# Performance work log

Hardware: AMD Instinct MI355X
Metric: run time of the kernel (lower is better)

The kernel has to match this reference:

```python
import jax, jax.numpy as jnp
import numpy as np

SIZE_IN = 4096
SIZE_OUT = 4096
STEPS = 8  # single-int steps variant of SparseLayer
BATCH = 8192


def _build_mask(size_in, size_out, steps):
    # Replicates the single-int `steps` branch of SparseLayer.__init__:
    # row i has ones at columns k*inp_el_counts + (i % inp_el_counts), k in [0, steps)
    inp_el_counts = size_in // steps
    rows = np.arange(size_out)
    count = rows % inp_el_counts                      # [size_out]
    cols = (np.arange(steps)[None, :] * inp_el_counts + count[:, None])  # [size_out, steps]
    mask = np.zeros((size_out, size_in), dtype=np.float32)
    mask[rows[:, None], cols] = 1.0
    return mask


def setup_inputs() -> dict:
    key = jax.random.key(0)
    kx, kw, kb = jax.random.split(key, 3)
    x = jax.random.normal(kx, (BATCH, SIZE_IN), dtype=jnp.float32)
    # kaiming_uniform_(a=sqrt(5)) -> uniform(-b, b) with b = sqrt(6/((1+5)*fan_in)) = 1/sqrt(fan_in)
    bound = 1.0 / np.sqrt(SIZE_IN)
    weights = jax.random.uniform(kw, (SIZE_OUT, SIZE_IN), minval=-bound, maxval=bound, dtype=jnp.float32)
    bias = jax.random.uniform(kb, (SIZE_OUT,), minval=-bound, maxval=bound, dtype=jnp.float32)
    mask = jnp.asarray(_build_mask(SIZE_IN, SIZE_OUT, STEPS))
    return {"x": x, "weights": weights, "bias": bias, "mask": mask}


def reference(x, weights, bias, mask):
    # out = x @ (W * mask)^T + b  ; mask is a fixed structured-sparsity pattern
    w = weights * mask                                  # [size_out, size_in]
    return jnp.einsum('bi,oi->bo', x, w) + bias         # [B, size_out]
```

## Files before the change

kernel.cpp:

```cpp
#include <hip/hip_runtime.h>

#define SIZE_IN   4096
#define SIZE_OUT  4096
#define STEPS     8
#define IEC       512
#define GROUPS    8
#define BATCH     8192

#define C0_TILE         128
#define ROWS_PER_BLOCK  8
#define THREADS         256

__global__ void sparse_compress_w(const float* __restrict__ W, float* __restrict__ wc) {
    int idx = blockIdx.x * blockDim.x + threadIdx.x;
    int c0 = idx & (IEC - 1);
    int k  = (idx >> 9) & (STEPS - 1);
    int g  = idx >> 12;
    int row = g * IEC + c0;
    int col = k * IEC + c0;
    wc[idx] = W[(size_t)row * SIZE_IN + col];
}

__global__ __launch_bounds__(THREADS) void sparse_mm(
        const float* __restrict__ x, const float* __restrict__ wc,
        const float* __restrict__ bias, float* __restrict__ out) {
    __shared__ float lw[GROUPS * STEPS * C0_TILE];
    const int bx  = blockIdx.x;
    const int by  = blockIdx.y;
    const int tid = threadIdx.x;

    const float4* wc4 = (const float4*)wc;
    float4*       lw4 = (float4*)lw;
    #pragma unroll
    for (int i = 0; i < 8; ++i) {
        int flat4 = i * THREADS + tid;
        int gk = flat4 >> 5;
        int c4 = flat4 & 31;
        lw4[flat4] = wc4[gk * (IEC / 4) + bx * (C0_TILE / 4) + c4];
    }
    __syncthreads();

    const int r    = tid >> 5;
    const int lane = tid & 31;
    const int b    = by * ROWS_PER_BLOCK + r;
    const int c0   = bx * C0_TILE + lane * 4;

    const float4* xrow = (const float4*)(x + (size_t)b * SIZE_IN);
    float4 xv[STEPS];
    #pragma unroll
    for (int k = 0; k < STEPS; ++k)
        xv[k] = xrow[(k * IEC + c0) >> 2];

    float4*       orow = (float4*)(out + (size_t)b * SIZE_OUT);
    const float4* b4   = (const float4*)bias;
    #pragma unroll
    for (int g = 0; g < GROUPS; ++g) {
        float4 acc = b4[(g * IEC + c0) >> 2];
        #pragma unroll
        for (int k = 0; k < STEPS; ++k) {
            const float4 w = *(const float4*)&lw[(g * STEPS + k) * C0_TILE + lane * 4];
            acc.x += xv[k].x * w.x;
            acc.y += xv[k].y * w.y;
            acc.z += xv[k].z * w.z;
            acc.w += xv[k].w * w.w;
        }
        orow[(g * IEC + c0) >> 2] = acc;
    }
}

extern "C" void kernel_launch(void* const* d_in, const int* in_sizes, int n_in,
                              void* d_out, int out_size, void* d_ws, size_t ws_size,
                              hipStream_t stream) {
    const float* x    = (const float*)d_in[0];
    const float* W    = (const float*)d_in[1];
    const float* bias = (const float*)d_in[2];
    float* out = (float*)d_out;
    float* wc  = (float*)d_ws;

    hipLaunchKernelGGL(sparse_compress_w,
                       dim3(GROUPS * STEPS * IEC / 256), dim3(256), 0, stream, W, wc);

    dim3 grid(IEC / C0_TILE, BATCH / ROWS_PER_BLOCK);
    hipLaunchKernelGGL(sparse_mm, grid, dim3(THREADS), 0, stream, x, wc, bias, out);
}
```

Baseline: 50.34 us.

## Make sparse_mm persistent over batch chunks and use nontemporal output stores

New measurement: 54.10 us. 1.07x slower.

```diff
diff --git a/kernel.cpp b/kernel.cpp
--- a/kernel.cpp
+++ b/kernel.cpp
@@ -10,6 +10,9 @@
 #define C0_TILE         128
 #define ROWS_PER_BLOCK  8
 #define THREADS         256
+#define GRID_Y          256
+
+typedef float f4 __attribute__((ext_vector_type(4)));
 
 __global__ void sparse_compress_w(const float* __restrict__ W, float* __restrict__ wc) {
     int idx = blockIdx.x * blockDim.x + threadIdx.x;
@@ -24,13 +27,11 @@
 __global__ __launch_bounds__(THREADS) void sparse_mm(
         const float* __restrict__ x, const float* __restrict__ wc,
         const float* __restrict__ bias, float* __restrict__ out) {
-    __shared__ float lw[GROUPS * STEPS * C0_TILE];
+    __shared__ f4 lw4[GROUPS * STEPS * (C0_TILE / 4)];
     const int bx  = blockIdx.x;
-    const int by  = blockIdx.y;
     const int tid = threadIdx.x;
 
-    const float4* wc4 = (const float4*)wc;
-    float4*       lw4 = (float4*)lw;
+    const f4* wc4 = (const f4*)wc;
     #pragma unroll
     for (int i = 0; i < 8; ++i) {
         int flat4 = i * THREADS + tid;
@@ -38,33 +39,37 @@
         int c4 = flat4 & 31;
         lw4[flat4] = wc4[gk * (IEC / 4) + bx * (C0_TILE / 4) + c4];
     }
-    __syncthreads();
 
     const int r    = tid >> 5;
     const int lane = tid & 31;
-    const int b    = by * ROWS_PER_BLOCK + r;
-    const int c0   = bx * C0_TILE + lane * 4;
 
-    const float4* xrow = (const float4*)(x + (size_t)b * SIZE_IN);
-    float4 xv[STEPS];
+    const f4* b4 = (const f4*)bias;
+    f4 bv[GROUPS];
     #pragma unroll
-    for (int k = 0; k < STEPS; ++k)
-        xv[k] = xrow[(k * IEC + c0) >> 2];
+    for (int g = 0; g < GROUPS; ++g)
+        bv[g] = b4[(g * IEC + bx * C0_TILE) / 4 + lane];
 
-    float4*       orow = (float4*)(out + (size_t)b * SIZE_OUT);
-    const float4* b4   = (const float4*)bias;
-    #pragma unroll
-    for (int g = 0; g < GROUPS; ++g) {
-        float4 acc = b4[(g * IEC + c0) >> 2];
+    __syncthreads();
+
+    for (int chunk = blockIdx.y; chunk < BATCH / ROWS_PER_BLOCK; chunk += GRID_Y) {
+        const int b = chunk * ROWS_PER_BLOCK + r;
+        const f4* xrow = (const f4*)(x + (size_t)b * SIZE_IN);
+        f4 xv[STEPS];
         #pragma unroll
-        for (int k = 0; k < STEPS; ++k) {
-            const float4 w = *(const float4*)&lw[(g * STEPS + k) * C0_TILE + lane * 4];
-            acc.x += xv[k].x * w.x;
-            acc.y += xv[k].y * w.y;
-            acc.z += xv[k].z * w.z;
-            acc.w += xv[k].w * w.w;
+        for (int k = 0; k < STEPS; ++k)
+            xv[k] = xrow[(k * IEC + bx * C0_TILE) / 4 + lane];
+
+        f4* orow = (f4*)(out + (size_t)b * SIZE_OUT);
+        #pragma unroll
+        for (int g = 0; g < GROUPS; ++g) {
+            f4 acc = bv[g];
+            #pragma unroll
+            for (int k = 0; k < STEPS; ++k) {
+                const f4 w = lw4[(g * STEPS + k) * (C0_TILE / 4) + lane];
+                acc += xv[k] * w;
+            }
+            __builtin_nontemporal_store(acc, &orow[(g * IEC + bx * C0_TILE) / 4 + lane]);
         }
-        orow[(g * IEC + c0) >> 2] = acc;
     }
 }
 
@@ -80,6 +85,6 @@
     hipLaunchKernelGGL(sparse_compress_w,
                        dim3(GROUPS * STEPS * IEC / 256), dim3(256), 0, stream, W, wc);
 
-    dim3 grid(IEC / C0_TILE, BATCH / ROWS_PER_BLOCK);
+    dim3 grid(IEC / C0_TILE, GRID_Y);
     hipLaunchKernelGGL(sparse_mm, grid, dim3(THREADS), 0, stream, x, wc, bias, out);
 }
```
